# Kernel tuning notes

Measured on AMD Instinct MI355X. Metric: run time of the kernel, lower is better.

## Reference

```python
import jax, jax.numpy as jnp
import numpy as np

B = 131072
D = 64
NUM_REL = 32


def setup_inputs() -> dict:
    key = jax.random.key(0)
    k1, k2, k3, k4 = jax.random.split(key, 4)
    embeds1 = jax.random.normal(k1, (B, D), dtype=jnp.float32)
    embeds2 = jax.random.normal(k2, (B, D), dtype=jnp.float32)
    rels = jax.random.randint(k3, (B,), 0, NUM_REL, dtype=jnp.int32)
    # learned relation table: one D*D matrix per relation type
    rel_embeds = jax.random.normal(k4, (NUM_REL, D * D), dtype=jnp.float32)
    return {"embeds1": embeds1, "embeds2": embeds2, "rels": rels,
            "rel_embeds": rel_embeds}


def reference(embeds1, embeds2, rels, rel_embeds):
    # gather per-sample relation matrices: [B, D, D]
    rel_mats = rel_embeds[rels].reshape(-1, D, D)
    # per-sample bilinear form: score_b = e1_b^T R_b e2_b  -> [B]
    e1R = jnp.einsum("bd,bde->be", embeds1, rel_mats)
    return (e1R * embeds2).sum(axis=1)
```

## Files before the change

### kernel.cpp

```cpp
#include <hip/hip_runtime.h>
#include <hip/hip_bf16.h>
#include <cstddef>

#define BB 131072
#define DD 64
#define NREL 32

#define CAP 4608
#define WPB (CAP / 64)
#define PERM_SLOTS (NREL * CAP)
#define NWAVE (NREL * WPB)

#define BLOCKS_SC 512

typedef __attribute__((ext_vector_type(8))) __bf16 bf16x8;
typedef __attribute__((ext_vector_type(16))) float f32x16;

__global__ __launch_bounds__(256) void prep_kernel(
    const float* __restrict__ relE, __bf16* __restrict__ RtH,
    __bf16* __restrict__ RtL, int* __restrict__ cursor) {
  __shared__ float sR[64 * 65];
  const int r = blockIdx.x;
  const int t = threadIdx.x;
  if (t == 0) cursor[r] = r * CAP;
#pragma unroll
  for (int i = 0; i < 16; ++i) {
    const int idx = i * 256 + t;
    const int d = idx >> 6, e = idx & 63;
    sR[e * 65 + d] = relE[(size_t)r * 4096 + idx];
  }
  __syncthreads();
#pragma unroll
  for (int i = 0; i < 16; ++i) {
    const int idx = i * 256 + t;
    const float x = sR[(idx >> 6) * 65 + (idx & 63)];
    const __bf16 hb = (__bf16)x;
    RtH[(size_t)r * 4096 + idx] = hb;
    RtL[(size_t)r * 4096 + idx] = (__bf16)(x - (float)hb);
  }
}

__global__ __launch_bounds__(256) void scatter_kernel(
    const int* __restrict__ rels, int* __restrict__ cursor,
    int* __restrict__ perm) {
  __shared__ int hist[NREL];
  __shared__ int base[NREL];
  const int t = threadIdx.x;
  if (t < NREL) hist[t] = 0;
  __syncthreads();
  const int s = blockIdx.x * 256 + t;
  const int rv = rels[s];
  const int rank = atomicAdd(&hist[rv], 1);
  __syncthreads();
  if (t < NREL) base[t] = atomicAdd(&cursor[t], hist[t]);
  __syncthreads();
  perm[base[rv] + rank] = s;
}

__global__ __launch_bounds__(64) void bilinear_mfma(
    const float* __restrict__ e1g, const float* __restrict__ e2g,
    const __bf16* __restrict__ RtH, const __bf16* __restrict__ RtL,
    const int* __restrict__ perm, const int* __restrict__ cursorEnd,
    float* __restrict__ out) {
  __shared__ float sP[64 * 33];
  const int lane = threadIdx.x;
  const int wb = blockIdx.x;
  const int r0 = wb / WPB;
  const int end = cursorEnd[r0];
  const int slotBase = wb * 64;
  if (slotBase >= end) return;
  const int slot = slotBase + lane;
  const int pk = perm[slot];
  const bool valid = slot < end;
  const int h = lane >> 5;
  const int l31 = lane & 31;

  int rowid[2];
  rowid[0] = __shfl(pk, l31) & 0x1FFFF;
  rowid[1] = __shfl(pk, 32 + l31) & 0x1FFFF;

  const __bf16* __restrict__ RH = RtH + (size_t)r0 * 4096;
  const __bf16* __restrict__ RL = RtL + (size_t)r0 * 4096;

  f32x16 acc[2][2];
#pragma unroll
  for (int ti = 0; ti < 2; ++ti)
#pragma unroll
    for (int tj = 0; tj < 2; ++tj)
#pragma unroll
      for (int i = 0; i < 16; ++i) acc[ti][tj][i] = 0.f;

#pragma unroll
  for (int kc = 0; kc < 4; ++kc) {
    bf16x8 aH[2], aL[2], bH[2], bL[2];
#pragma unroll
    for (int ti = 0; ti < 2; ++ti) {
      const float* ap = e1g + (size_t)rowid[ti] * DD + kc * 16 + 8 * h;
      const float4 x0 = *(const float4*)(ap);
      const float4 x1 = *(const float4*)(ap + 4);
      const float xs[8] = {x0.x, x0.y, x0.z, x0.w, x1.x, x1.y, x1.z, x1.w};
#pragma unroll
      for (int j = 0; j < 8; ++j) {
        const __bf16 hb = (__bf16)xs[j];
        aH[ti][j] = hb;
        aL[ti][j] = (__bf16)(xs[j] - (float)hb);
      }
    }
#pragma unroll
    for (int tj = 0; tj < 2; ++tj) {
      const size_t bo = (size_t)(32 * tj + l31) * DD + kc * 16 + 8 * h;
      bH[tj] = *(const bf16x8*)(RH + bo);
      bL[tj] = *(const bf16x8*)(RL + bo);
    }
#pragma unroll
    for (int ti = 0; ti < 2; ++ti)
#pragma unroll
      for (int tj = 0; tj < 2; ++tj) {
        acc[ti][tj] = __builtin_amdgcn_mfma_f32_32x32x16_bf16(aH[ti], bH[tj], acc[ti][tj], 0, 0, 0);
        acc[ti][tj] = __builtin_amdgcn_mfma_f32_32x32x16_bf16(aH[ti], bL[tj], acc[ti][tj], 0, 0, 0);
        acc[ti][tj] = __builtin_amdgcn_mfma_f32_32x32x16_bf16(aL[ti], bH[tj], acc[ti][tj], 0, 0, 0);
      }
  }

#pragma unroll
  for (int ti = 0; ti < 2; ++ti)
#pragma unroll
    for (int g = 0; g < 4; ++g)
#pragma unroll
      for (int q = 0; q < 4; ++q) {
        const int reg = g * 4 + q;
        const int rbase = 32 * ti + q + 8 * g;
        const int s0 = __builtin_amdgcn_readlane(pk, rbase) & 0x1FFFF;
        const int s1 = __builtin_amdgcn_readlane(pk, rbase + 4) & 0x1FFFF;
        const int bs = h ? s1 : s0;
        const float* er = e2g + (size_t)bs * DD + l31;
        const float v = fmaf(acc[ti][0][reg], er[0], acc[ti][1][reg] * er[32]);
        sP[(rbase + 4 * h) * 33 + l31] = v;
      }
  __syncthreads();
  float sc = 0.f;
#pragma unroll
  for (int c = 0; c < 32; ++c) sc += sP[lane * 33 + c];
  if (valid) out[pk] = sc;
}

extern "C" void kernel_launch(void* const* d_in, const int* in_sizes, int n_in,
                              void* d_out, int out_size, void* d_ws, size_t ws_size,
                              hipStream_t stream) {
  const float* e1 = (const float*)d_in[0];
  const float* e2 = (const float*)d_in[1];
  const int* rels = (const int*)d_in[2];
  const float* relE = (const float*)d_in[3];
  float* out = (float*)d_out;

  int* perm = (int*)d_ws;
  int* cursor = perm + PERM_SLOTS;
  __bf16* RtH = (__bf16*)(cursor + NREL);
  __bf16* RtL = RtH + NREL * 4096;

  prep_kernel<<<NREL, 256, 0, stream>>>(relE, RtH, RtL, cursor);
  scatter_kernel<<<BLOCKS_SC, 256, 0, stream>>>(rels, cursor, perm);
  bilinear_mfma<<<NWAVE, 64, 0, stream>>>(e1, e2, RtH, RtL, perm, cursor, out);
}
```

Before: 122.7 us.

## Drop relation prep kernel; split relation matrices to bf16 inside the MFMA kernel

Removes the separate prep kernel that transposed and split each relation matrix into bf16 high and low parts. The main kernel now reads the fp32 relation matrix directly with strided column loads and does the split itself. Cursors are zeroed with a memset, padded to separate cache lines, and made relative to each relation, and the scatter uses 512-thread blocks. This saves one kernel launch and a pass over the relation table, at the cost of redundant conversion and less coalesced B-operand loads in every wave.

New measurement: 122.8 us. About the same (+0.0%).

```diff
diff --git a/kernel.cpp b/kernel.cpp
--- a/kernel.cpp
+++ b/kernel.cpp
@@ -9,38 +9,15 @@
 #define CAP 4608
 #define WPB (CAP / 64)
 #define PERM_SLOTS (NREL * CAP)
-#define NWAVE (NREL * WPB)
 
-#define BLOCKS_SC 512
+#define SCB 256
+#define SCT 512
+#define CSTRIDE 16
 
 typedef __attribute__((ext_vector_type(8))) __bf16 bf16x8;
 typedef __attribute__((ext_vector_type(16))) float f32x16;
 
-__global__ __launch_bounds__(256) void prep_kernel(
-    const float* __restrict__ relE, __bf16* __restrict__ RtH,
-    __bf16* __restrict__ RtL, int* __restrict__ cursor) {
-  __shared__ float sR[64 * 65];
-  const int r = blockIdx.x;
-  const int t = threadIdx.x;
-  if (t == 0) cursor[r] = r * CAP;
-#pragma unroll
-  for (int i = 0; i < 16; ++i) {
-    const int idx = i * 256 + t;
-    const int d = idx >> 6, e = idx & 63;
-    sR[e * 65 + d] = relE[(size_t)r * 4096 + idx];
-  }
-  __syncthreads();
-#pragma unroll
-  for (int i = 0; i < 16; ++i) {
-    const int idx = i * 256 + t;
-    const float x = sR[(idx >> 6) * 65 + (idx & 63)];
-    const __bf16 hb = (__bf16)x;
-    RtH[(size_t)r * 4096 + idx] = hb;
-    RtL[(size_t)r * 4096 + idx] = (__bf16)(x - (float)hb);
-  }
-}
-
-__global__ __launch_bounds__(256) void scatter_kernel(
+__global__ __launch_bounds__(SCT) void scatter_atomic(
     const int* __restrict__ rels, int* __restrict__ cursor,
     int* __restrict__ perm) {
   __shared__ int hist[NREL];
@@ -48,39 +25,34 @@
   const int t = threadIdx.x;
   if (t < NREL) hist[t] = 0;
   __syncthreads();
-  const int s = blockIdx.x * 256 + t;
+  const int s = blockIdx.x * SCT + t;
   const int rv = rels[s];
   const int rank = atomicAdd(&hist[rv], 1);
   __syncthreads();
-  if (t < NREL) base[t] = atomicAdd(&cursor[t], hist[t]);
+  if (t < NREL) base[t] = atomicAdd(&cursor[t * CSTRIDE], hist[t]);
   __syncthreads();
-  perm[base[rv] + rank] = s;
+  perm[rv * CAP + base[rv] + rank] = s;
 }
 
 __global__ __launch_bounds__(64) void bilinear_mfma(
     const float* __restrict__ e1g, const float* __restrict__ e2g,
-    const __bf16* __restrict__ RtH, const __bf16* __restrict__ RtL,
-    const int* __restrict__ perm, const int* __restrict__ cursorEnd,
-    float* __restrict__ out) {
+    const float* __restrict__ relE, const int* __restrict__ perm,
+    const int* __restrict__ cursor, float* __restrict__ out) {
   __shared__ float sP[64 * 33];
   const int lane = threadIdx.x;
-  const int wb = blockIdx.x;
-  const int r0 = wb / WPB;
-  const int end = cursorEnd[r0];
-  const int slotBase = wb * 64;
-  if (slotBase >= end) return;
-  const int slot = slotBase + lane;
-  const int pk = perm[slot];
+  const int r0 = blockIdx.y;
+  const int end = cursor[r0 * CSTRIDE];
+  const int s0i = blockIdx.x * 64;
+  if (s0i >= end) return;
+  const int slot = s0i + lane;
   const bool valid = slot < end;
+  const int pk = perm[r0 * CAP + slot] & 0x1FFFF;
   const int h = lane >> 5;
   const int l31 = lane & 31;
+  const int rowid0 = __shfl(pk, l31);
+  const int rowid1 = __shfl(pk, 32 + l31);
 
-  int rowid[2];
-  rowid[0] = __shfl(pk, l31) & 0x1FFFF;
-  rowid[1] = __shfl(pk, 32 + l31) & 0x1FFFF;
-
-  const __bf16* __restrict__ RH = RtH + (size_t)r0 * 4096;
-  const __bf16* __restrict__ RL = RtL + (size_t)r0 * 4096;
+  const float* __restrict__ R = relE + (size_t)r0 * (DD * DD);
 
   f32x16 acc[2][2];
 #pragma unroll
@@ -95,7 +67,8 @@
     bf16x8 aH[2], aL[2], bH[2], bL[2];
 #pragma unroll
     for (int ti = 0; ti < 2; ++ti) {
-      const float* ap = e1g + (size_t)rowid[ti] * DD + kc * 16 + 8 * h;
+      const float* ap =
+          e1g + (size_t)(ti ? rowid1 : rowid0) * DD + kc * 16 + 8 * h;
       const float4 x0 = *(const float4*)(ap);
       const float4 x1 = *(const float4*)(ap + 4);
       const float xs[8] = {x0.x, x0.y, x0.z, x0.w, x1.x, x1.y, x1.z, x1.w};
@@ -108,9 +81,14 @@
     }
 #pragma unroll
     for (int tj = 0; tj < 2; ++tj) {
-      const size_t bo = (size_t)(32 * tj + l31) * DD + kc * 16 + 8 * h;
-      bH[tj] = *(const bf16x8*)(RH + bo);
-      bL[tj] = *(const bf16x8*)(RL + bo);
+      const float* q = R + (size_t)(kc * 16 + 8 * h) * DD + 32 * tj + l31;
+#pragma unroll
+      for (int j = 0; j < 8; ++j) {
+        const float x = q[(size_t)j * DD];
+        const __bf16 hb = (__bf16)x;
+        bH[tj][j] = hb;
+        bL[tj][j] = (__bf16)(x - (float)hb);
+      }
     }
 #pragma unroll
     for (int ti = 0; ti < 2; ++ti)
@@ -130,8 +108,8 @@
       for (int q = 0; q < 4; ++q) {
         const int reg = g * 4 + q;
         const int rbase = 32 * ti + q + 8 * g;
-        const int s0 = __builtin_amdgcn_readlane(pk, rbase) & 0x1FFFF;
-        const int s1 = __builtin_amdgcn_readlane(pk, rbase + 4) & 0x1FFFF;
+        const int s0 = __builtin_amdgcn_readlane(pk, rbase);
+        const int s1 = __builtin_amdgcn_readlane(pk, rbase + 4);
         const int bs = h ? s1 : s0;
         const float* er = e2g + (size_t)bs * DD + l31;
         const float v = fmaf(acc[ti][0][reg], er[0], acc[ti][1][reg] * er[32]);
@@ -155,10 +133,9 @@
 
   int* perm = (int*)d_ws;
   int* cursor = perm + PERM_SLOTS;
-  __bf16* RtH = (__bf16*)(cursor + NREL);
-  __bf16* RtL = RtH + NREL * 4096;
 
-  prep_kernel<<<NREL, 256, 0, stream>>>(relE, RtH, RtL, cursor);
-  scatter_kernel<<<BLOCKS_SC, 256, 0, stream>>>(rels, cursor, perm);
-  bilinear_mfma<<<NWAVE, 64, 0, stream>>>(e1, e2, RtH, RtL, perm, cursor, out);
+  hipMemsetAsync(cursor, 0, NREL * CSTRIDE * sizeof(int), stream);
+  scatter_atomic<<<SCB, SCT, 0, stream>>>(rels, cursor, perm);
+  bilinear_mfma<<<dim3(WPB, NREL), 64, 0, stream>>>(e1, e2, relE, perm, cursor,
+                                                    out);
 }
```
